# Kernel tuning notes

Hardware: AMD Instinct MI355X
Metric: run time of the kernel (lower is better)

## Reference

```python
import jax, jax.numpy as jnp
import numpy as np

B, N, QD, H, D = 2, 2048, 1152, 16, 72
INNER = H * D
RETAIN_RATE = 0.4  # layer_count in [4, 64] branch
N_KEEP = int(N * RETAIN_RATE)
N_PRUNE = N - N_KEEP
SCALE = D ** (-0.5)


def setup_inputs() -> dict:
    key = jax.random.key(0)
    ks = jax.random.split(key, 6)
    s = 0.02
    return {
        "x": jax.random.normal(ks[0], (B, N, QD), jnp.float32),
        "Wq": jax.random.normal(ks[1], (QD, INNER), jnp.float32) * s,
        "Wk": jax.random.normal(ks[2], (QD, INNER), jnp.float32) * s,
        "Wv": jax.random.normal(ks[3], (QD, INNER), jnp.float32) * s,
        "Wo": jax.random.normal(ks[4], (INNER, QD), jnp.float32) * s,
        "bo": jnp.zeros((QD,), jnp.float32),
    }


def reference(x, Wq, Wk, Wv, Wo, bo):
    b = x.shape[0]
    # self-attention: context = x
    q = (x @ Wq).reshape(b, N, H, D).transpose(0, 2, 1, 3)  # [b,H,N,D]
    k = (x @ Wk).reshape(b, N, H, D).transpose(0, 2, 1, 3)
    v = (x @ Wv).reshape(b, N, H, D).transpose(0, 2, 1, 3)

    # ---- WPR pruning pass: full attention map, mean over heads ----
    logits = jnp.einsum('bhnd,bhmd->bhnm', q, k) * SCALE  # [b,H,N,N]
    M = jax.nn.softmax(logits, axis=-1)
    attn = M.mean(axis=1)  # [b,N,N]

    # 5-step power iteration: dist = (1/N) @ attn^5
    dist = jnp.full((b, 1, N), 1.0 / N, dtype=attn.dtype)
    for _ in range(5):
        dist = dist @ attn
    importance = dist[:, 0]  # [b,N]

    _, imp_inds = jax.lax.top_k(importance, N_KEEP)
    _, prune_inds = jax.lax.top_k(-importance, N_PRUNE)
    # boolean-mask selection in torch returns rows in ascending index order
    sorted_imp = jnp.sort(imp_inds, axis=1)      # [b,N_KEEP]
    sorted_prune = jnp.sort(prune_inds, axis=1)  # [b,N_PRUNE]

    selected_rows = jnp.take_along_axis(attn, sorted_imp[:, :, None], axis=1)  # [b,N_KEEP,N]
    max_inds = jnp.argmax(selected_rows, axis=1)  # [b,N]: most-attending retained row per token
    sim_inds = jnp.take_along_axis(max_inds, sorted_prune, axis=1)  # [b,N_PRUNE]

    # ---- attention among retained tokens only ----
    gi = sorted_imp[:, None, :, None]  # broadcast gather index
    q_r = jnp.take_along_axis(q, gi, axis=2)  # [b,H,N_KEEP,D]
    k_r = jnp.take_along_axis(k, gi, axis=2)
    v_r = jnp.take_along_axis(v, gi, axis=2)
    attn_r = jax.nn.softmax(jnp.einsum('bhnd,bhmd->bhnm', q_r, k_r) * SCALE, axis=-1)
    out_r = jnp.einsum('bhnm,bhmd->bhnd', attn_r, v_r)  # [b,H,N_KEEP,D]
    out_r = out_r.transpose(0, 2, 1, 3).reshape(b, N_KEEP, INNER)

    # similarity-based recovery for pruned tokens
    out_p = jnp.take_along_axis(out_r, sim_inds[:, :, None], axis=1)  # [b,N_PRUNE,INNER]

    bidx = jnp.arange(b)[:, None]
    out = jnp.zeros((b, N, INNER), out_r.dtype)
    out = out.at[bidx, sorted_imp].set(out_r)
    out = out.at[bidx, sorted_prune].set(out_p)

    return out @ Wo + bo
```

## Files before the change

### kernel.cpp

```cpp
#include <hip/hip_runtime.h>

namespace {
constexpr int B = 2;
constexpr int N = 2048;
constexpr int QD = 1152;
constexpr int H = 16;
constexpr int D = 72;
constexpr int INNER = 1152;
constexpr int NKEEP = 819;
constexpr int PSL = 8;
constexpr int ILEN = N / PSL;
constexpr int DP = 80;
constexpr int LSTR = 88;
}

#define FINF __builtin_inff()
#define SCALE 0.11785113019775793f

typedef __attribute__((ext_vector_type(8))) __bf16 bf16x8;
typedef __attribute__((ext_vector_type(16))) float f32x16;
typedef __attribute__((ext_vector_type(8))) short short8;

__device__ __forceinline__ f32x16 mfma_bf16(bf16x8 a, bf16x8 b, f32x16 c) {
  return __builtin_amdgcn_mfma_f32_32x32x16_bf16(a, b, c, 0, 0, 0);
}
__device__ __forceinline__ short f2bf(float x) {
  unsigned u = __float_as_uint(x);
  unsigned r = (u + 0x7fffu + ((u >> 16) & 1u)) >> 16;
  return (short)r;
}
__device__ __forceinline__ float bf2f(short b) {
  return __uint_as_float(((unsigned)(unsigned short)b) << 16);
}

__global__ __launch_bounds__(256) void k_xsplit(
    const float* __restrict__ X, short* __restrict__ Xh, short* __restrict__ Xl,
    int total)
{
  int g = blockIdx.x * 256 + threadIdx.x;
  if (g >= total) return;
  float v = X[g];
  short hb = f2bf(v);
  Xh[g] = hb;
  Xl[g] = f2bf(v - bf2f(hb));
}

__global__ __launch_bounds__(256) void k_wsplitT(
    const float* __restrict__ W, short* __restrict__ WTh, short* __restrict__ WTl)
{
  __shared__ float tile[64][65];
  const int tid = threadIdx.x;
  const int k0 = blockIdx.y * 64, n0 = blockIdx.x * 64;
  {
    int r = tid >> 2, c0 = (tid & 3) * 16;
#pragma unroll
    for (int j = 0; j < 16; j += 4) {
      float4 v = *(const float4*)&W[(size_t)(k0 + r) * 1152 + n0 + c0 + j];
      tile[r][c0 + j] = v.x; tile[r][c0 + j + 1] = v.y;
      tile[r][c0 + j + 2] = v.z; tile[r][c0 + j + 3] = v.w;
    }
  }
  __syncthreads();
  for (int e = tid; e < 4096; e += 256) {
    int nr = e >> 6, kc = e & 63;
    float v = tile[kc][nr];
    short hb = f2bf(v);
    WTh[(size_t)(n0 + nr) * 1152 + k0 + kc] = hb;
    WTl[(size_t)(n0 + nr) * 1152 + k0 + kc] = f2bf(v - bf2f(hb));
  }
}

__global__ __launch_bounds__(256, 2) void k_pgemm3(
    const short* __restrict__ Ah_g, const short* __restrict__ Al_g,
    const short* __restrict__ Bh_g, const short* __restrict__ Bl_g,
    short* __restrict__ QKV0)
{
  constexpr int LK = 40;
  __shared__ short AhS[256 * LK], AlS[256 * LK];
  __shared__ short BhS[128 * LK], BlS[128 * LK];
  const int tid = threadIdx.x;
  const int wv = tid >> 6, ln = tid & 63;
  const int col = ln & 31, hi = ln >> 5;
  const int wm = wv >> 1, wn = wv & 1;
  const int m0 = blockIdx.y * 256, n0 = blockIdx.x * 128;
  f32x16 acc[4][2];
#pragma unroll
  for (int mi = 0; mi < 4; ++mi)
#pragma unroll
    for (int ni = 0; ni < 2; ++ni)
#pragma unroll
      for (int r = 0; r < 16; ++r) acc[mi][ni][r] = 0.f;

  for (int kt = 0; kt < 1152; kt += 32) {
    __syncthreads();
    for (int e = tid; e < 1024; e += 256) {
      int r = e >> 2, c4 = e & 3;
      size_t sa = (size_t)(m0 + r) * 1152 + kt + c4 * 8;
      *(float4*)&AhS[r * LK + c4 * 8] = *(const float4*)(Ah_g + sa);
      *(float4*)&AlS[r * LK + c4 * 8] = *(const float4*)(Al_g + sa);
    }
    for (int e = tid; e < 512; e += 256) {
      int r = e >> 2, c4 = e & 3;
      size_t sb = (size_t)(n0 + r) * 1152 + kt + c4 * 8;
      *(float4*)&BhS[r * LK + c4 * 8] = *(const float4*)(Bh_g + sb);
      *(float4*)&BlS[r * LK + c4 * 8] = *(const float4*)(Bl_g + sb);
    }
    __syncthreads();
#pragma unroll
    for (int kc = 0; kc < 2; ++kc) {
      bf16x8 ah[4], al[4], bh[2], bl[2];
#pragma unroll
      for (int mi = 0; mi < 4; ++mi) {
        int r = wm * 128 + mi * 32 + col;
        ah[mi] = *(const bf16x8*)&AhS[r * LK + kc * 16 + hi * 8];
        al[mi] = *(const bf16x8*)&AlS[r * LK + kc * 16 + hi * 8];
      }
#pragma unroll
      for (int ni = 0; ni < 2; ++ni) {
        int r = wn * 64 + ni * 32 + col;
        bh[ni] = *(const bf16x8*)&BhS[r * LK + kc * 16 + hi * 8];
        bl[ni] = *(const bf16x8*)&BlS[r * LK + kc * 16 + hi * 8];
      }
#pragma unroll
      for (int mi = 0; mi < 4; ++mi)
#pragma unroll
        for (int ni = 0; ni < 2; ++ni) {
          acc[mi][ni] = mfma_bf16(ah[mi], bh[ni], acc[mi][ni]);
          acc[mi][ni] = mfma_bf16(ah[mi], bl[ni], acc[mi][ni]);
          acc[mi][ni] = mfma_bf16(al[mi], bh[ni], acc[mi][ni]);
        }
    }
  }
  const size_t S = (size_t)65536 * 80;
#pragma unroll
  for (int mi = 0; mi < 4; ++mi)
#pragma unroll
    for (int ni = 0; ni < 2; ++ni)
#pragma unroll
      for (int r = 0; r < 16; ++r) {
        int m = m0 + wm * 128 + mi * 32 + (r & 3) + 8 * (r >> 2) + 4 * hi;
        int c = n0 + wn * 64 + ni * 32 + col;
        int which = c / 1152, cm = c - which * 1152;
        int hh = cm / 72, dd = cm - hh * 72;
        int b = m >> 11, nn = m & 2047;
        size_t idx = (((size_t)(b * 16 + hh)) * 2048 + nn) * 80 + dd;
        float v = acc[mi][ni][r];
        short hb = f2bf(v);
        short* OH = QKV0 + (size_t)which * 2 * S;
        OH[idx] = hb;
        OH[S + idx] = f2bf(v - bf2f(hb));
      }
}

__global__ __launch_bounds__(256, 2) void k_stats3(
    const short* __restrict__ Qh, const short* __restrict__ Ql,
    const short* __restrict__ Kh, const short* __restrict__ Kl,
    float* __restrict__ inv_out)
{
  __shared__ __align__(16) short kh[64 * LSTR];
  __shared__ __align__(16) short kl[64 * LSTR];
  const int tid = threadIdx.x;
  const int wv = tid >> 6, ln = tid & 63;
  const int col = ln & 31, hi = ln >> 5;
  const int q0 = blockIdx.x * 256;
  const int h = blockIdx.y, b = blockIdx.z;
  const size_t bhbase = (size_t)(b * H + h) * N * DP;

  bf16x8 qfh[2][5], qfl[2][5];
#pragma unroll
  for (int mi = 0; mi < 2; ++mi) {
    const size_t rb = bhbase + (size_t)(q0 + wv * 64 + mi * 32 + col) * DP + hi * 8;
#pragma unroll
    for (int d = 0; d < 5; ++d) {
      qfh[mi][d] = *(const bf16x8*)(const void*)(Qh + rb + d * 16);
      qfl[mi][d] = *(const bf16x8*)(const void*)(Ql + rb + d * 16);
    }
  }
  float s[2][16];
#pragma unroll
  for (int mi = 0; mi < 2; ++mi)
#pragma unroll
    for (int r = 0; r < 16; ++r) s[mi][r] = 0.f;

  for (int kt = 0; kt < N; kt += 64) {
    __syncthreads();
    for (int c = tid; c < 640; c += 256) {
      int r = c / 10, cc = c - r * 10;
      *(float4*)(void*)(kh + r * LSTR + cc * 8) =
          *(const float4*)(const void*)(Kh + bhbase + (size_t)(kt + r) * DP + cc * 8);
      *(float4*)(void*)(kl + r * LSTR + cc * 8) =
          *(const float4*)(const void*)(Kl + bhbase + (size_t)(kt + r) * DP + cc * 8);
    }
    __syncthreads();
    f32x16 z[2][2];
#pragma unroll
    for (int mi = 0; mi < 2; ++mi)
#pragma unroll
      for (int rn = 0; rn < 2; ++rn)
#pragma unroll
        for (int r = 0; r < 16; ++r) z[mi][rn][r] = 0.f;
#pragma unroll
    for (int d = 0; d < 5; ++d) {
      const int boff = d * 16 + hi * 8;
      bf16x8 bh0 = *(const bf16x8*)(const void*)(kh + col * LSTR + boff);
      bf16x8 bl0 = *(const bf16x8*)(const void*)(kl + col * LSTR + boff);
      bf16x8 bh1 = *(const bf16x8*)(const void*)(kh + (32 + col) * LSTR + boff);
      bf16x8 bl1 = *(const bf16x8*)(const void*)(kl + (32 + col) * LSTR + boff);
#pragma unroll
      for (int mi = 0; mi < 2; ++mi) {
        z[mi][0] = mfma_bf16(qfh[mi][d], bh0, z[mi][0]);
        z[mi][0] = mfma_bf16(qfh[mi][d], bl0, z[mi][0]);
        z[mi][0] = mfma_bf16(qfl[mi][d], bh0, z[mi][0]);
        z[mi][1] = mfma_bf16(qfh[mi][d], bh1, z[mi][1]);
        z[mi][1] = mfma_bf16(qfh[mi][d], bl1, z[mi][1]);
        z[mi][1] = mfma_bf16(qfl[mi][d], bh1, z[mi][1]);
      }
    }
#pragma unroll
    for (int mi = 0; mi < 2; ++mi)
#pragma unroll
      for (int r = 0; r < 16; ++r)
        s[mi][r] += __expf(z[mi][0][r] * SCALE) + __expf(z[mi][1][r] * SCALE);
  }
#pragma unroll
  for (int mi = 0; mi < 2; ++mi)
#pragma unroll
    for (int r = 0; r < 16; ++r) {
      float v = s[mi][r];
#pragma unroll
      for (int o = 1; o < 32; o <<= 1) v += __shfl_xor(v, o);
      if (col == 0) {
        int row = q0 + wv * 64 + mi * 32 + ((r & 3) + ((r >> 2) << 3) + (hi << 2));
        inv_out[(size_t)(b * H + h) * N + row] = 1.0f / v;
      }
    }
}

__global__ __launch_bounds__(256, 2) void k_attn3(
    const short* __restrict__ Qh, const short* __restrict__ Ql,
    const short* __restrict__ Kh, const short* __restrict__ Kl,
    const float* __restrict__ inv_in, float* __restrict__ attn)
{
  __shared__ __align__(16) short kh[64 * LSTR];
  __shared__ __align__(16) short kl[64 * LSTR];
  __shared__ float invs[256];
  const int tid = threadIdx.x;
  const int wv = tid >> 6, ln = tid & 63;
  const int col = ln & 31, hi = ln >> 5;
  const int k0 = blockIdx.x * 64, q0 = blockIdx.y * 256, b = blockIdx.z;

  f32x16 pa[2][2];
#pragma unroll
  for (int mi = 0; mi < 2; ++mi)
#pragma unroll
    for (int rn = 0; rn < 2; ++rn)
#pragma unroll
      for (int r = 0; r < 16; ++r) pa[mi][rn][r] = 0.f;

  for (int h = 0; h < H; ++h) {
    const size_t bhbase = (size_t)(b * H + h) * N * DP;
    __syncthreads();
    for (int c = tid; c < 640; c += 256) {
      int r = c / 10, cc = c - r * 10;
      *(float4*)(void*)(kh + r * LSTR + cc * 8) =
          *(const float4*)(const void*)(Kh + bhbase + (size_t)(k0 + r) * DP + cc * 8);
      *(float4*)(void*)(kl + r * LSTR + cc * 8) =
          *(const float4*)(const void*)(Kl + bhbase + (size_t)(k0 + r) * DP + cc * 8);
    }
    invs[tid] = inv_in[(size_t)(b * H + h) * N + q0 + tid];
    __syncthreads();

    f32x16 z[2][2];
#pragma unroll
    for (int mi = 0; mi < 2; ++mi)
#pragma unroll
      for (int rn = 0; rn < 2; ++rn)
#pragma unroll
        for (int r = 0; r < 16; ++r) z[mi][rn][r] = 0.f;

#pragma unroll
    for (int d = 0; d < 5; ++d) {
      const int boff = d * 16 + hi * 8;
      bf16x8 bh0 = *(const bf16x8*)(const void*)(kh + col * LSTR + boff);
      bf16x8 bl0 = *(const bf16x8*)(const void*)(kl + col * LSTR + boff);
      bf16x8 bh1 = *(const bf16x8*)(const void*)(kh + (32 + col) * LSTR + boff);
      bf16x8 bl1 = *(const bf16x8*)(const void*)(kl + (32 + col) * LSTR + boff);
      bf16x8 qh0 = *(const bf16x8*)(const void*)(Qh + bhbase + (size_t)(q0 + wv * 64 + col) * DP + boff);
      bf16x8 ql0 = *(const bf16x8*)(const void*)(Ql + bhbase + (size_t)(q0 + wv * 64 + col) * DP + boff);
      bf16x8 qh1 = *(const bf16x8*)(const void*)(Qh + bhbase + (size_t)(q0 + wv * 64 + 32 + col) * DP + boff);
      bf16x8 ql1 = *(const bf16x8*)(const void*)(Ql + bhbase + (size_t)(q0 + wv * 64 + 32 + col) * DP + boff);
      z[0][0] = mfma_bf16(qh0, bh0, z[0][0]);
      z[0][0] = mfma_bf16(qh0, bl0, z[0][0]);
      z[0][0] = mfma_bf16(ql0, bh0, z[0][0]);
      z[0][1] = mfma_bf16(qh0, bh1, z[0][1]);
      z[0][1] = mfma_bf16(qh0, bl1, z[0][1]);
      z[0][1] = mfma_bf16(ql0, bh1, z[0][1]);
      z[1][0] = mfma_bf16(qh1, bh0, z[1][0]);
      z[1][0] = mfma_bf16(qh1, bl0, z[1][0]);
      z[1][0] = mfma_bf16(ql1, bh0, z[1][0]);
      z[1][1] = mfma_bf16(qh1, bh1, z[1][1]);
      z[1][1] = mfma_bf16(qh1, bl1, z[1][1]);
      z[1][1] = mfma_bf16(ql1, bh1, z[1][1]);
    }
#pragma unroll
    for (int mi = 0; mi < 2; ++mi)
#pragma unroll
      for (int r = 0; r < 16; ++r) {
        const int rloc = wv * 64 + mi * 32 + (r & 3) + ((r >> 2) << 3) + (hi << 2);
        const float iv = invs[rloc];
        pa[mi][0][r] += __expf(z[mi][0][r] * SCALE) * iv;
        pa[mi][1][r] += __expf(z[mi][1][r] * SCALE) * iv;
      }
  }
  const float invH = 1.0f / H;
#pragma unroll
  for (int mi = 0; mi < 2; ++mi)
#pragma unroll
    for (int r = 0; r < 16; ++r) {
      const int row = q0 + wv * 64 + mi * 32 + (r & 3) + ((r >> 2) << 3) + (hi << 2);
      attn[((size_t)b * N + row) * N + k0 + col] = pa[mi][0][r] * invH;
      attn[((size_t)b * N + row) * N + k0 + 32 + col] = pa[mi][1][r] * invH;
    }
}

__global__ __launch_bounds__(256) void k_power(
    const float* __restrict__ attn, const float* __restrict__ din,
    float* __restrict__ partial, int first)
{
  int g = blockIdx.x * 256 + threadIdx.x;
  int sy = blockIdx.y;
  int b = g / N, j = g % N;
  const float* ab = attn + (size_t)b * N * N;
  int i0 = sy * ILEN;
  float sum = 0.f;
  if (first) {
    for (int i = i0; i < i0 + ILEN; ++i) sum += ab[(size_t)i * N + j];
    sum *= (1.0f / N);
  } else {
    const float* db = din + b * N;
    for (int i = i0; i < i0 + ILEN; ++i) sum += db[i] * ab[(size_t)i * N + j];
  }
  partial[(size_t)sy * (B * N) + g] = sum;
}

__global__ __launch_bounds__(256) void k_powred(
    const float* __restrict__ partial, float* __restrict__ dout)
{
  int g = blockIdx.x * 256 + threadIdx.x;
  if (g >= B * N) return;
  float s = 0.f;
  for (int sy = 0; sy < PSL; ++sy) s += partial[(size_t)sy * (B * N) + g];
  dout[g] = s;
}

__global__ __launch_bounds__(1024) void k_partition(
    const float* __restrict__ imp, int* __restrict__ sorted_imp,
    int* __restrict__ keepflag, int* __restrict__ s_map)
{
  __shared__ float v[N];
  __shared__ int   id[N];
  __shared__ int   kf[N];
  __shared__ int   ps[N];
  const int tid = threadIdx.x;
  const int b = blockIdx.x;
  for (int i = tid; i < N; i += 1024) { v[i] = imp[b * N + i]; id[i] = i; }
  for (int k = 2; k <= N; k <<= 1) {
    for (int j = k >> 1; j > 0; j >>= 1) {
      __syncthreads();
      for (int i = tid; i < N; i += 1024) {
        int ixj = i ^ j;
        if (ixj > i) {
          bool up = ((i & k) == 0);
          float va = v[i], vb = v[ixj];
          int ia = id[i], ib = id[ixj];
          bool b_before_a = (vb > va) || (vb == va && ib < ia);
          if (b_before_a == up) { v[i] = vb; v[ixj] = va; id[i] = ib; id[ixj] = ia; }
        }
      }
    }
  }
  __syncthreads();
  for (int i = tid; i < N; i += 1024) kf[id[i]] = (i < NKEEP) ? 1 : 0;
  __syncthreads();
  for (int i = tid; i < N; i += 1024) ps[i] = kf[i];
  for (int off = 1; off < N; off <<= 1) {
    __syncthreads();
    int t0 = (tid >= off) ? ps[tid - off] : 0;
    int i1 = tid + 1024;
    int t1 = ps[i1 - off];
    __syncthreads();
    ps[tid] += t0;
    ps[i1] += t1;
  }
  __syncthreads();
  for (int i = tid; i < N; i += 1024) {
    int excl = ps[i] - kf[i];
    keepflag[b * N + i] = kf[i];
    if (kf[i]) { sorted_imp[b * NKEEP + excl] = i; s_map[b * N + i] = excl; }
  }
}

__global__ __launch_bounds__(256) void k_argmax(
    const float* __restrict__ attn, const int* __restrict__ sorted_imp,
    const int* __restrict__ keepflag, int* __restrict__ s_map)
{
  __shared__ int imp_s[NKEEP];
  const int tid = threadIdx.x;
  const int g = blockIdx.x * 256 + tid;
  const int b = g / N, n = g % N;
  for (int i = tid; i < NKEEP; i += 256) imp_s[i] = sorted_imp[b * NKEEP + i];
  __syncthreads();
  const float* ab = attn + (size_t)b * N * N;
  float best = -FINF; int bi = 0;
  for (int k = 0; k < NKEEP; ++k) {
    float val = ab[(size_t)imp_s[k] * N + n];
    if (val > best) { best = val; bi = k; }
  }
  if (!keepflag[g]) s_map[g] = bi;
}

__global__ __launch_bounds__(256, 2) void k_rfused(
    const short* __restrict__ Qh, const short* __restrict__ Ql,
    const short* __restrict__ Kh, const short* __restrict__ Kl,
    const short* __restrict__ Vh, const int* __restrict__ sorted_imp,
    short* __restrict__ Yh, short* __restrict__ Yl)
{
  constexpr int LK = 88;
  constexpr int VTS = 72;
  __shared__ __align__(16) short KhS[64 * LK];
  __shared__ __align__(16) short KlS[64 * LK];
  __shared__ __align__(16) short VhS[64 * LK];
  __shared__ __align__(16) short VT[72 * VTS];
  __shared__ int imp[NKEEP];
  const int tid = threadIdx.x;
  const int wv = tid >> 6, ln = tid & 63;
  const int col = ln & 31, hi = ln >> 5;
  const int b = blockIdx.z, h = blockIdx.y, q0 = blockIdx.x * 128;
  const size_t bh80 = (size_t)(b * H + h) * N * DP;
  for (int i = tid; i < NKEEP; i += 256) imp[i] = sorted_imp[b * NKEEP + i];
  __syncthreads();
  int qr = q0 + wv * 32 + col;
  int qi = imp[qr < NKEEP ? qr : NKEEP - 1];
  bf16x8 qfh[5], qfl[5];
  {
    const size_t qb = bh80 + (size_t)qi * DP + hi * 8;
#pragma unroll
    for (int d = 0; d < 5; ++d) {
      qfh[d] = *(const bf16x8*)(const void*)(Qh + qb + d * 16);
      qfl[d] = *(const bf16x8*)(const void*)(Ql + qb + d * 16);
    }
  }
  float denom = 0.f;
  f32x16 oacc[3];
#pragma unroll
  for (int nc = 0; nc < 3; ++nc)
#pragma unroll
    for (int r = 0; r < 16; ++r) oacc[nc][r] = 0.f;

  for (int kt = 0; kt < 832; kt += 64) {
    for (int e = tid; e < 640; e += 256) {
      int r = e / 10, cc = e - r * 10;
      int kv = kt + r;
      float4 vkh, vkl, vvh;
      if (kv < NKEEP) {
        size_t sb = bh80 + (size_t)imp[kv] * DP + cc * 8;
        vkh = *(const float4*)(const void*)(Kh + sb);
        vkl = *(const float4*)(const void*)(Kl + sb);
        vvh = *(const float4*)(const void*)(Vh + sb);
      } else {
        vkh = make_float4(0.f, 0.f, 0.f, 0.f); vkl = vkh; vvh = vkh;
      }
      *(float4*)(void*)&KhS[r * LK + cc * 8] = vkh;
      *(float4*)(void*)&KlS[r * LK + cc * 8] = vkl;
      *(float4*)(void*)&VhS[r * LK + cc * 8] = vvh;
    }
    __syncthreads();
    f32x16 z[2];
#pragma unroll
    for (int rn = 0; rn < 2; ++rn)
#pragma unroll
      for (int r = 0; r < 16; ++r) z[rn][r] = 0.f;
#pragma unroll
    for (int d = 0; d < 5; ++d) {
      const int boff = d * 16 + hi * 8;
#pragma unroll
      for (int rn = 0; rn < 2; ++rn) {
        bf16x8 kfh = *(const bf16x8*)(const void*)(KhS + (rn * 32 + col) * LK + boff);
        bf16x8 kfl = *(const bf16x8*)(const void*)(KlS + (rn * 32 + col) * LK + boff);
        z[rn] = mfma_bf16(kfh, qfh[d], z[rn]);
        z[rn] = mfma_bf16(kfh, qfl[d], z[rn]);
        z[rn] = mfma_bf16(kfl, qfh[d], z[rn]);
      }
    }
    for (int e = tid; e < 576; e += 256) {
      int dd = e % 72, k8 = e / 72;
      short8 t;
#pragma unroll
      for (int j = 0; j < 8; ++j) t[j] = VhS[(k8 * 8 + j) * LK + dd];
      *(short8*)(void*)&VT[dd * VTS + k8 * 8] = t;
    }
    const bool full = (kt + 64 <= NKEEP);
#pragma unroll
    for (int rn = 0; rn < 2; ++rn) {
      int kvb = kt + rn * 32 + 4 * hi;
#pragma unroll
      for (int r = 0; r < 16; ++r) {
        float pe = __expf(z[rn][r] * SCALE);
        if (!full) {
          int kv = kvb + (r & 3) + 8 * (r >> 2);
          pe = (kv < NKEEP) ? pe : 0.f;
        }
        z[rn][r] = pe;
        denom += pe;
      }
    }
    __syncthreads();
#pragma unroll
    for (int rn = 0; rn < 2; ++rn) {
#pragma unroll
      for (int kc = 0; kc < 2; ++kc) {
        unsigned p0, p1, p2, p3;
        asm("v_cvt_pk_bf16_f32 %0, %1, %2" : "=v"(p0) : "v"(z[rn][8 * kc + 0]), "v"(z[rn][8 * kc + 1]));
        asm("v_cvt_pk_bf16_f32 %0, %1, %2" : "=v"(p1) : "v"(z[rn][8 * kc + 2]), "v"(z[rn][8 * kc + 3]));
        asm("v_cvt_pk_bf16_f32 %0, %1, %2" : "=v"(p2) : "v"(z[rn][8 * kc + 4]), "v"(z[rn][8 * kc + 5]));
        asm("v_cvt_pk_bf16_f32 %0, %1, %2" : "=v"(p3) : "v"(z[rn][8 * kc + 6]), "v"(z[rn][8 * kc + 7]));
        unsigned othA = hi ? p0 : p2, othB = hi ? p1 : p3;
        unsigned swA = (unsigned)__shfl_xor((int)othA, 32);
        unsigned swB = (unsigned)__shfl_xor((int)othB, 32);
        union { unsigned u[4]; bf16x8 v; } pf;
        pf.u[0] = hi ? swA : p0; pf.u[1] = hi ? swB : p1;
        pf.u[2] = hi ? p2 : swA; pf.u[3] = hi ? p3 : swB;
        const int kb = rn * 32 + kc * 16 + hi * 8;
#pragma unroll
        for (int nc = 0; nc < 3; ++nc) {
          int dr = nc * 32 + col; if (dr > 71) dr = 71;
          bf16x8 vf = *(const bf16x8*)(const void*)(VT + dr * VTS + kb);
          oacc[nc] = mfma_bf16(pf.v, vf, oacc[nc]);
        }
      }
    }
  }
  denom += __shfl_xor(denom, 32);
  float invd = 1.0f / denom;
#pragma unroll
  for (int r = 0; r < 16; ++r) {
    int cr = (r & 3) + 8 * (r >> 2) + 4 * hi;
    int q = q0 + wv * 32 + cr;
    float dv = __shfl(invd, cr);
    if (q < NKEEP) {
#pragma unroll
      for (int nc = 0; nc < 3; ++nc) {
        int dd = nc * 32 + col;
        if (dd < 72) {
          float v = oacc[nc][r] * dv;
          size_t idx = ((size_t)b * NKEEP + q) * 1152 + h * 72 + dd;
          short hb = f2bf(v);
          Yh[idx] = hb;
          Yl[idx] = f2bf(v - bf2f(hb));
        }
      }
    }
  }
}

__global__ __launch_bounds__(256, 2) void k_pgemm(
    const short* __restrict__ Ah_g, const short* __restrict__ Al_g,
    const short* __restrict__ Bh_g, const short* __restrict__ Bl_g,
    float* __restrict__ OutF, const float* __restrict__ bias,
    int Mtot)
{
  constexpr int LK = 40;
  __shared__ short AhS[128 * LK], AlS[128 * LK], BhS[128 * LK], BlS[128 * LK];
  const int tid = threadIdx.x;
  const int wv = tid >> 6, ln = tid & 63;
  const int col = ln & 31, hi = ln >> 5;
  const int wm = wv >> 1, wn = wv & 1;
  const int m0 = blockIdx.y * 128, n0 = blockIdx.x * 128;
  f32x16 acc[2][2];
#pragma unroll
  for (int mi = 0; mi < 2; ++mi)
#pragma unroll
    for (int ni = 0; ni < 2; ++ni)
#pragma unroll
      for (int r = 0; r < 16; ++r) acc[mi][ni][r] = 0.f;

  for (int kt = 0; kt < 1152; kt += 32) {
    __syncthreads();
    for (int e = tid; e < 512; e += 256) {
      int r = e >> 2, c4 = e & 3;
      int ra = m0 + r; if (ra >= Mtot) ra = Mtot - 1;
      size_t sa = (size_t)ra * 1152 + kt + c4 * 8;
      *(float4*)&AhS[r * LK + c4 * 8] = *(const float4*)(Ah_g + sa);
      *(float4*)&AlS[r * LK + c4 * 8] = *(const float4*)(Al_g + sa);
      size_t sb = (size_t)(n0 + r) * 1152 + kt + c4 * 8;
      *(float4*)&BhS[r * LK + c4 * 8] = *(const float4*)(Bh_g + sb);
      *(float4*)&BlS[r * LK + c4 * 8] = *(const float4*)(Bl_g + sb);
    }
    __syncthreads();
#pragma unroll
    for (int kc = 0; kc < 2; ++kc) {
      bf16x8 ah[2], al[2], bh[2], bl[2];
#pragma unroll
      for (int mi = 0; mi < 2; ++mi) {
        int r = wm * 64 + mi * 32 + col;
        ah[mi] = *(const bf16x8*)&AhS[r * LK + kc * 16 + hi * 8];
        al[mi] = *(const bf16x8*)&AlS[r * LK + kc * 16 + hi * 8];
      }
#pragma unroll
      for (int ni = 0; ni < 2; ++ni) {
        int r = wn * 64 + ni * 32 + col;
        bh[ni] = *(const bf16x8*)&BhS[r * LK + kc * 16 + hi * 8];
        bl[ni] = *(const bf16x8*)&BlS[r * LK + kc * 16 + hi * 8];
      }
#pragma unroll
      for (int mi = 0; mi < 2; ++mi)
#pragma unroll
        for (int ni = 0; ni < 2; ++ni) {
          acc[mi][ni] = mfma_bf16(ah[mi], bh[ni], acc[mi][ni]);
          acc[mi][ni] = mfma_bf16(ah[mi], bl[ni], acc[mi][ni]);
          acc[mi][ni] = mfma_bf16(al[mi], bh[ni], acc[mi][ni]);
        }
    }
  }
#pragma unroll
  for (int mi = 0; mi < 2; ++mi)
#pragma unroll
    for (int ni = 0; ni < 2; ++ni)
#pragma unroll
      for (int r = 0; r < 16; ++r) {
        int m = m0 + wm * 64 + mi * 32 + (r & 3) + 8 * (r >> 2) + 4 * hi;
        int c = n0 + wn * 64 + ni * 32 + col;
        if (m < Mtot) OutF[(size_t)m * 1152 + c] = acc[mi][ni][r] + bias[c];
      }
}

__global__ __launch_bounds__(256) void k_scatter(
    const float* __restrict__ Y, const int* __restrict__ s_map,
    float* __restrict__ out)
{
  size_t g = (size_t)blockIdx.x * 256 + threadIdx.x;
  if (g >= (size_t)B * N * QD) return;
  int c = (int)(g % QD);
  int n_ = (int)((g / QD) % N);
  int b = (int)(g / ((size_t)N * QD));
  int src = s_map[b * N + n_];
  out[g] = Y[((size_t)b * NKEEP + src) * QD + c];
}

extern "C" void kernel_launch(void* const* d_in, const int* in_sizes, int n_in,
                              void* d_out, int out_size, void* d_ws, size_t ws_size,
                              hipStream_t stream)
{
  const float* x  = (const float*)d_in[0];
  const float* Wq = (const float*)d_in[1];
  const float* Wk = (const float*)d_in[2];
  const float* Wv = (const float*)d_in[3];
  const float* Wo = (const float*)d_in[4];
  const float* bo = (const float*)d_in[5];
  float* out = (float*)d_out;

  char* ws = (char*)d_ws;
  size_t off = 0;
  auto alloc = [&](size_t bytes) -> void* {
    void* p = ws + off;
    off = (off + bytes + 255) & ~(size_t)255;
    return p;
  };
  const int ROWS = B * H * N;
  const size_t XEL = (size_t)B * N * QD;
  const size_t WEL = (size_t)QD * INNER;
  short* xh   = (short*)alloc(sizeof(short) * XEL);
  short* xl   = (short*)alloc(sizeof(short) * XEL);
  short* WTh  = (short*)alloc(sizeof(short) * WEL * 3);
  short* WTl  = (short*)alloc(sizeof(short) * WEL * 3);
  short* Qhb  = (short*)alloc(sizeof(short) * (size_t)ROWS * DP);
  short* Qlb  = (short*)alloc(sizeof(short) * (size_t)ROWS * DP);
  short* Khb  = (short*)alloc(sizeof(short) * (size_t)ROWS * DP);
  short* Klb  = (short*)alloc(sizeof(short) * (size_t)ROWS * DP);
  short* Vhb  = (short*)alloc(sizeof(short) * (size_t)ROWS * DP);
  short* Vlb  = (short*)alloc(sizeof(short) * (size_t)ROWS * DP);
  float* attn = (float*)alloc(sizeof(float) * (size_t)B * N * N);
  float* inv  = (float*)alloc(sizeof(float) * (size_t)ROWS);
  float* d0   = (float*)alloc(sizeof(float) * B * N);
  float* d1   = (float*)alloc(sizeof(float) * B * N);
  float* partial = (float*)alloc(sizeof(float) * PSL * B * N);
  int* sorted_imp = (int*)alloc(sizeof(int) * B * NKEEP);
  int* keepflag   = (int*)alloc(sizeof(int) * B * N);
  int* s_map      = (int*)alloc(sizeof(int) * B * N);
  (void)Vlb;
  short* Yh = xh;
  short* Yl = xh + (size_t)B * NKEEP * INNER;
  float* Y  = (float*)xl;

  dim3 blk(256);

  k_xsplit<<<dim3(((int)XEL + 255) / 256), blk, 0, stream>>>(x, xh, xl, (int)XEL);
  dim3 wg(QD / 64, QD / 64);
  k_wsplitT<<<wg, blk, 0, stream>>>(Wq, WTh, WTl);
  k_wsplitT<<<wg, blk, 0, stream>>>(Wk, WTh + WEL, WTl + WEL);
  k_wsplitT<<<wg, blk, 0, stream>>>(Wv, WTh + 2 * WEL, WTl + 2 * WEL);

  hipMemsetAsync(Qhb, 0, sizeof(short) * (size_t)ROWS * DP * 6, stream);

  k_pgemm3<<<dim3(3 * INNER / 128, (B * N) / 256), blk, 0, stream>>>(
      xh, xl, WTh, WTl, Qhb);

  k_wsplitT<<<wg, blk, 0, stream>>>(Wo, WTh, WTl);

  k_stats3<<<dim3(N / 256, H, B), blk, 0, stream>>>(Qhb, Qlb, Khb, Klb, inv);
  k_attn3<<<dim3(N / 64, N / 256, B), blk, 0, stream>>>(Qhb, Qlb, Khb, Klb, inv, attn);

  k_power<<<dim3(B * N / 256, PSL), blk, 0, stream>>>(attn, nullptr, partial, 1);
  k_powred<<<dim3(B * N / 256), blk, 0, stream>>>(partial, d0);
  float* src = d0; float* dst = d1;
  for (int it = 1; it < 5; ++it) {
    k_power<<<dim3(B * N / 256, PSL), blk, 0, stream>>>(attn, src, partial, 0);
    k_powred<<<dim3(B * N / 256), blk, 0, stream>>>(partial, dst);
    float* t = src; src = dst; dst = t;
  }

  k_partition<<<dim3(B), dim3(1024), 0, stream>>>(src, sorted_imp, keepflag, s_map);
  k_argmax<<<dim3(B * N / 256), blk, 0, stream>>>(attn, sorted_imp, keepflag, s_map);

  k_rfused<<<dim3((NKEEP + 127) / 128, H, B), blk, 0, stream>>>(
      Qhb, Qlb, Khb, Klb, Vhb, sorted_imp, Yh, Yl);

  k_pgemm<<<dim3(QD / 128, (B * NKEEP + 127) / 128), blk, 0, stream>>>(
      Yh, Yl, WTh, WTl, Y, bo, B * NKEEP);
  k_scatter<<<dim3((int)(((size_t)B * N * QD + 255) / 256)), blk, 0, stream>>>(Y, s_map, out);
}
```

Before: 589.8 us.

## Register-prefetch next tiles in projection GEMM and attention kernels, shrink GEMM tile

The QKV projection GEMM moves from 256-row to 128-row tiles with launch bounds of three blocks per SM. It prefetches the next K-slice into registers while MFMAs run on the current shared-memory tile. The stats and attention-map kernels get the same register prefetch of the next K tile or next head's K and inverse sums. The power-iteration split factor also rises from 8 to 32. The aim is to hide global-load latency behind compute and raise occupancy and grid size, at the cost of more registers, more reloads of B tiles, and more partial sums to reduce.

```diff
diff --git a/kernel.cpp b/kernel.cpp
--- a/kernel.cpp
+++ b/kernel.cpp
@@ -8,7 +8,7 @@
 constexpr int D = 72;
 constexpr int INNER = 1152;
 constexpr int NKEEP = 819;
-constexpr int PSL = 8;
+constexpr int PSL = 32;
 constexpr int ILEN = N / PSL;
 constexpr int DP = 80;
 constexpr int LSTR = 88;
@@ -70,48 +70,64 @@
   }
 }
 
-__global__ __launch_bounds__(256, 2) void k_pgemm3(
+__global__ __launch_bounds__(256, 3) void k_pgemm3(
     const short* __restrict__ Ah_g, const short* __restrict__ Al_g,
     const short* __restrict__ Bh_g, const short* __restrict__ Bl_g,
     short* __restrict__ QKV0)
 {
   constexpr int LK = 40;
-  __shared__ short AhS[256 * LK], AlS[256 * LK];
+  __shared__ short AhS[128 * LK], AlS[128 * LK];
   __shared__ short BhS[128 * LK], BlS[128 * LK];
   const int tid = threadIdx.x;
   const int wv = tid >> 6, ln = tid & 63;
   const int col = ln & 31, hi = ln >> 5;
   const int wm = wv >> 1, wn = wv & 1;
-  const int m0 = blockIdx.y * 256, n0 = blockIdx.x * 128;
-  f32x16 acc[4][2];
-#pragma unroll
-  for (int mi = 0; mi < 4; ++mi)
+  const int m0 = blockIdx.y * 128, n0 = blockIdx.x * 128;
+  const int sr = tid >> 2, sc = (tid & 3) * 8;
+  float4 rah[2], ral[2], rbh[2], rbl[2];
+
+  auto LOAD = [&](int kt) {
+#pragma unroll
+    for (int s = 0; s < 2; ++s) {
+      int r = sr + s * 64;
+      size_t sa = (size_t)(m0 + r) * 1152 + kt + sc;
+      rah[s] = *(const float4*)(const void*)(Ah_g + sa);
+      ral[s] = *(const float4*)(const void*)(Al_g + sa);
+      size_t sb = (size_t)(n0 + r) * 1152 + kt + sc;
+      rbh[s] = *(const float4*)(const void*)(Bh_g + sb);
+      rbl[s] = *(const float4*)(const void*)(Bl_g + sb);
+    }
+  };
+  auto STORE = [&]() {
+#pragma unroll
+    for (int s = 0; s < 2; ++s) {
+      int r = sr + s * 64;
+      *(float4*)(void*)&AhS[r * LK + sc] = rah[s];
+      *(float4*)(void*)&AlS[r * LK + sc] = ral[s];
+      *(float4*)(void*)&BhS[r * LK + sc] = rbh[s];
+      *(float4*)(void*)&BlS[r * LK + sc] = rbl[s];
+    }
+  };
+
+  f32x16 acc[2][2];
+#pragma unroll
+  for (int mi = 0; mi < 2; ++mi)
 #pragma unroll
     for (int ni = 0; ni < 2; ++ni)
 #pragma unroll
       for (int r = 0; r < 16; ++r) acc[mi][ni][r] = 0.f;
 
+  LOAD(0);
+  STORE();
   for (int kt = 0; kt < 1152; kt += 32) {
     __syncthreads();
-    for (int e = tid; e < 1024; e += 256) {
-      int r = e >> 2, c4 = e & 3;
-      size_t sa = (size_t)(m0 + r) * 1152 + kt + c4 * 8;
-      *(float4*)&AhS[r * LK + c4 * 8] = *(const float4*)(Ah_g + sa);
-      *(float4*)&AlS[r * LK + c4 * 8] = *(const float4*)(Al_g + sa);
-    }
-    for (int e = tid; e < 512; e += 256) {
-      int r = e >> 2, c4 = e & 3;
-      size_t sb = (size_t)(n0 + r) * 1152 + kt + c4 * 8;
-      *(float4*)&BhS[r * LK + c4 * 8] = *(const float4*)(Bh_g + sb);
-      *(float4*)&BlS[r * LK + c4 * 8] = *(const float4*)(Bl_g + sb);
-    }
-    __syncthreads();
+    if (kt + 32 < 1152) LOAD(kt + 32);
 #pragma unroll
     for (int kc = 0; kc < 2; ++kc) {
-      bf16x8 ah[4], al[4], bh[2], bl[2];
-#pragma unroll
-      for (int mi = 0; mi < 4; ++mi) {
-        int r = wm * 128 + mi * 32 + col;
+      bf16x8 ah[2], al[2], bh[2], bl[2];
+#pragma unroll
+      for (int mi = 0; mi < 2; ++mi) {
+        int r = wm * 64 + mi * 32 + col;
         ah[mi] = *(const bf16x8*)&AhS[r * LK + kc * 16 + hi * 8];
         al[mi] = *(const bf16x8*)&AlS[r * LK + kc * 16 + hi * 8];
       }
@@ -122,7 +138,7 @@
         bl[ni] = *(const bf16x8*)&BlS[r * LK + kc * 16 + hi * 8];
       }
 #pragma unroll
-      for (int mi = 0; mi < 4; ++mi)
+      for (int mi = 0; mi < 2; ++mi)
 #pragma unroll
         for (int ni = 0; ni < 2; ++ni) {
           acc[mi][ni] = mfma_bf16(ah[mi], bh[ni], acc[mi][ni]);
@@ -130,15 +146,18 @@
           acc[mi][ni] = mfma_bf16(al[mi], bh[ni], acc[mi][ni]);
         }
     }
-  }
+    __syncthreads();
+    if (kt + 32 < 1152) STORE();
+  }
+
   const size_t S = (size_t)65536 * 80;
 #pragma unroll
-  for (int mi = 0; mi < 4; ++mi)
+  for (int mi = 0; mi < 2; ++mi)
 #pragma unroll
     for (int ni = 0; ni < 2; ++ni)
 #pragma unroll
       for (int r = 0; r < 16; ++r) {
-        int m = m0 + wm * 128 + mi * 32 + (r & 3) + 8 * (r >> 2) + 4 * hi;
+        int m = m0 + wm * 64 + mi * 32 + (r & 3) + 8 * (r >> 2) + 4 * hi;
         int c = n0 + wn * 64 + ni * 32 + col;
         int which = c / 1152, cm = c - which * 1152;
         int hh = cm / 72, dd = cm - hh * 72;
@@ -182,16 +201,37 @@
 #pragma unroll
     for (int r = 0; r < 16; ++r) s[mi][r] = 0.f;
 
+  float4 rkh[3], rkl[3];
+  auto LOADK = [&](int kt) {
+#pragma unroll
+    for (int ss = 0; ss < 3; ++ss) {
+      int e = ss * 256 + tid;
+      if (e < 640) {
+        int r = e / 10, cc = e - r * 10;
+        size_t sb = bhbase + (size_t)(kt + r) * DP + cc * 8;
+        rkh[ss] = *(const float4*)(const void*)(Kh + sb);
+        rkl[ss] = *(const float4*)(const void*)(Kl + sb);
+      }
+    }
+  };
+  auto STOREK = [&]() {
+#pragma unroll
+    for (int ss = 0; ss < 3; ++ss) {
+      int e = ss * 256 + tid;
+      if (e < 640) {
+        int r = e / 10, cc = e - r * 10;
+        *(float4*)(void*)(kh + r * LSTR + cc * 8) = rkh[ss];
+        *(float4*)(void*)(kl + r * LSTR + cc * 8) = rkl[ss];
+      }
+    }
+  };
+
+  LOADK(0);
   for (int kt = 0; kt < N; kt += 64) {
     __syncthreads();
-    for (int c = tid; c < 640; c += 256) {
-      int r = c / 10, cc = c - r * 10;
-      *(float4*)(void*)(kh + r * LSTR + cc * 8) =
-          *(const float4*)(const void*)(Kh + bhbase + (size_t)(kt + r) * DP + cc * 8);
-      *(float4*)(void*)(kl + r * LSTR + cc * 8) =
-          *(const float4*)(const void*)(Kl + bhbase + (size_t)(kt + r) * DP + cc * 8);
-    }
-    __syncthreads();
+    STOREK();
+    __syncthreads();
+    if (kt + 64 < N) LOADK(kt + 64);
     f32x16 z[2][2];
 #pragma unroll
     for (int mi = 0; mi < 2; ++mi)
@@ -257,19 +297,43 @@
 #pragma unroll
       for (int r = 0; r < 16; ++r) pa[mi][rn][r] = 0.f;
 
+  float4 rkh[3], rkl[3];
+  float rin;
+  auto LOADH = [&](int h) {
+    const size_t hb = (size_t)(b * H + h) * N * DP;
+#pragma unroll
+    for (int ss = 0; ss < 3; ++ss) {
+      int e = ss * 256 + tid;
+      if (e < 640) {
+        int r = e / 10, cc = e - r * 10;
+        size_t sb = hb + (size_t)(k0 + r) * DP + cc * 8;
+        rkh[ss] = *(const float4*)(const void*)(Kh + sb);
+        rkl[ss] = *(const float4*)(const void*)(Kl + sb);
+      }
+    }
+    rin = inv_in[(size_t)(b * H + h) * N + q0 + tid];
+  };
+  auto STOREH = [&]() {
+#pragma unroll
+    for (int ss = 0; ss < 3; ++ss) {
+      int e = ss * 256 + tid;
+      if (e < 640) {
+        int r = e / 10, cc = e - r * 10;
+        *(float4*)(void*)(kh + r * LSTR + cc * 8) = rkh[ss];
+        *(float4*)(void*)(kl + r * LSTR + cc * 8) = rkl[ss];
+      }
+    }
+    invs[tid] = rin;
+  };
+
+  LOADH(0);
   for (int h = 0; h < H; ++h) {
+    __syncthreads();
+    STOREH();
+    __syncthreads();
+    if (h + 1 < H) LOADH(h + 1);
+
     const size_t bhbase = (size_t)(b * H + h) * N * DP;
-    __syncthreads();
-    for (int c = tid; c < 640; c += 256) {
-      int r = c / 10, cc = c - r * 10;
-      *(float4*)(void*)(kh + r * LSTR + cc * 8) =
-          *(const float4*)(const void*)(Kh + bhbase + (size_t)(k0 + r) * DP + cc * 8);
-      *(float4*)(void*)(kl + r * LSTR + cc * 8) =
-          *(const float4*)(const void*)(Kl + bhbase + (size_t)(k0 + r) * DP + cc * 8);
-    }
-    invs[tid] = inv_in[(size_t)(b * H + h) * N + q0 + tid];
-    __syncthreads();
-
     f32x16 z[2][2];
 #pragma unroll
     for (int mi = 0; mi < 2; ++mi)
@@ -702,7 +766,7 @@
 
   hipMemsetAsync(Qhb, 0, sizeof(short) * (size_t)ROWS * DP * 6, stream);
 
-  k_pgemm3<<<dim3(3 * INNER / 128, (B * N) / 256), blk, 0, stream>>>(
+  k_pgemm3<<<dim3(3 * INNER / 128, (B * N) / 128), blk, 0, stream>>>(
       xh, xl, WTh, WTl, Qhb);
 
   k_wsplitT<<<wg, blk, 0, stream>>>(Wo, WTh, WTl);
```

Measured after the change: 980.7 us. 1.66x slower.
